# Optimization experiments

Measured on AMD Instinct MI355X. Metric: run time of the kernel, lower is better.

Reference implementation:

```python
import jax, jax.numpy as jnp
import numpy as np


def _proj(W, b, x):
    # 1x1 conv == per-pixel GEMM over channels: [O,C] x [B,C,H,W] -> [B,O,H,W]
    return jnp.einsum('oc,bchw->bohw', W, x) + b[None, :, None, None]


def _cross(src, ctx, Wq, bq, Wk, bk, Wv, bv):
    # queries from src, keys/values from ctx; returns [B,C,H,W]
    B, C, H, W = src.shape
    HW = H * W
    q = _proj(Wq, bq, src).reshape(B, -1, HW)   # [B, C//8, HW]
    k = _proj(Wk, bk, ctx).reshape(B, -1, HW)   # [B, C//8, HW]
    v = _proj(Wv, bv, ctx).reshape(B, C, HW)    # [B, C,    HW]
    # attn[b,i,j] = softmax_j( q[b,:,i] . k[b,:,j] )
    attn = jax.nn.softmax(jnp.einsum('bci,bcj->bij', q, k), axis=-1)
    out = jnp.einsum('bcj,bij->bci', v, attn)   # [B, C, HW]
    return out.reshape(B, C, H, W)


def setup_inputs() -> dict:
    key = jax.random.key(0)
    ks = jax.random.split(key, 8)
    dim = 256
    B, H, W = 4, 64, 64
    return {
        'x': jax.random.normal(ks[0], (B, dim, H, W), jnp.float32),
        'y': jax.random.normal(ks[1], (B, dim, H, W), jnp.float32),
        'Wq': jax.random.normal(ks[2], (dim // 8, dim), jnp.float32) * 0.05,
        'bq': jax.random.normal(ks[3], (dim // 8,), jnp.float32) * 0.05,
        'Wk': jax.random.normal(ks[4], (dim // 8, dim), jnp.float32) * 0.05,
        'bk': jax.random.normal(ks[5], (dim // 8,), jnp.float32) * 0.05,
        'Wv': jax.random.normal(ks[6], (dim, dim), jnp.float32) * 0.05,
        'bv': jax.random.normal(ks[7], (dim,), jnp.float32) * 0.05,
    }


def reference(x, y, Wq, bq, Wk, bk, Wv, bv):
    outx = _cross(x, y, Wq, bq, Wk, bk, Wv, bv)  # x queries attend to y
    outy = _cross(y, x, Wq, bq, Wk, bk, Wv, bv)  # y queries attend to x
    return (outx, outy)
```

## Files before the change

kernel.cpp:

```cpp
#include <hip/hip_runtime.h>

#define BB 4
#define CC 256
#define DD 32
#define SS 4096

typedef __bf16 bf16;
typedef __bf16 bf16x8 __attribute__((ext_vector_type(8)));
typedef __bf16 bf16x4 __attribute__((ext_vector_type(4)));
typedef float f32x4 __attribute__((ext_vector_type(4)));
typedef unsigned int u32;
typedef unsigned short u16;

#define Q_OFF  0
#define K_OFF  1048576
#define V_OFF  2097152
#define WB_OFF 10485760

static __device__ __forceinline__ u32 pack2(float lo, float hi) {
    bf16 a = (bf16)lo, b = (bf16)hi;
    u16 ua = __builtin_bit_cast(u16, a), ub = __builtin_bit_cast(u16, b);
    return (u32)ua | ((u32)ub << 16);
}

__global__ __launch_bounds__(256) void convert_w_kernel(
    const float* __restrict__ Wq, const float* __restrict__ Wk,
    const float* __restrict__ Wv, bf16* __restrict__ wb)
{
    const int gid = blockIdx.x*256 + threadIdx.x;
    const int idx = gid*8;
    const int o = idx >> 8, cc = idx & 255;
    const float* row = (o < 32) ? (Wq + (size_t)o*CC)
                     : (o < 64) ? (Wk + (size_t)(o-32)*CC)
                                : (Wv + (size_t)(o-64)*CC);
    const float4 a = *(const float4*)(row + cc);
    const float4 c = *(const float4*)(row + cc + 4);
    bf16x8 pk;
    pk[0]=(bf16)a.x; pk[1]=(bf16)a.y; pk[2]=(bf16)a.z; pk[3]=(bf16)a.w;
    pk[4]=(bf16)c.x; pk[5]=(bf16)c.y; pk[6]=(bf16)c.z; pk[7]=(bf16)c.w;
    *(bf16x8*)(wb + idx) = pk;
}

__global__ __launch_bounds__(256, 2) void proj_all_kernel(
    const float* __restrict__ x, const float* __restrict__ y,
    const bf16* __restrict__ wb,
    const float* __restrict__ bq, const float* __restrict__ bk,
    const float* __restrict__ bv,
    bf16* __restrict__ qout, bf16* __restrict__ kout, bf16* __restrict__ vout)
{
    __shared__ __align__(16) char smem[2*5120];
    bf16* xT  = (bf16*)smem;
    u32*  xTw = (u32*)smem;

    const int t    = threadIdx.x;
    const int lane = t & 63;
    const int w    = t >> 6;
    const int ln   = lane & 15;
    const int quad = lane >> 4;

    const int bid  = blockIdx.x;
    const int dirb = bid & 7;
    const int src  = dirb >> 2;
    const int b    = dirb & 3;
    const int i0   = (bid >> 3) * 64;
    const float* in = src ? y : x;
    const float* xbase = in + (size_t)b*CC*SS + i0;

    const int cp = t >> 4;
    const int pq = (t & 15) * 4;

    float bias[5];
    #pragma unroll
    for (int nbl = 0; nbl < 5; ++nbl) {
        const int o = 80*w + nbl*16 + ln;
        bias[nbl] = (o < 32) ? bq[o] : (o < 64) ? bk[o-32] : bv[o-64];
    }
    f32x4 acc[4][5];
    #pragma unroll
    for (int mb = 0; mb < 4; ++mb)
        #pragma unroll
        for (int nbl = 0; nbl < 5; ++nbl)
            acc[mb][nbl] = (f32x4){bias[nbl], bias[nbl], bias[nbl], bias[nbl]};

    const bf16* wrow = wb + (size_t)(80*w + ln)*CC + quad*8;
    bf16x8 bf[5];
    #pragma unroll
    for (int nbl = 0; nbl < 5; ++nbl)
        bf[nbl] = *(const bf16x8*)(wrow + (size_t)nbl*16*CC);

    {
        const float* r0 = xbase + (size_t)(2*cp)*SS + pq;
        const float4 a0 = *(const float4*)r0;
        const float4 a1 = *(const float4*)(r0 + SS);
        xTw[(pq+0)*20 + cp] = pack2(a0.x, a1.x);
        xTw[(pq+1)*20 + cp] = pack2(a0.y, a1.y);
        xTw[(pq+2)*20 + cp] = pack2(a0.z, a1.z);
        xTw[(pq+3)*20 + cp] = pack2(a0.w, a1.w);
    }
    float4 a0, a1;
    {
        const float* r1 = xbase + (size_t)(32 + 2*cp)*SS + pq;
        a0 = *(const float4*)r1;
        a1 = *(const float4*)(r1 + SS);
    }
    __syncthreads();

    for (int n = 0; n < 8; ++n) {
        bf16x8 af[4];
        #pragma unroll
        for (int mb = 0; mb < 4; ++mb)
            af[mb] = *(const bf16x8*)(xT + (n&1)*2560 + (mb*16 + ln)*40 + quad*8);
        if (n < 7) {
            u32* dst = xTw + ((n+1)&1)*1280;
            dst[(pq+0)*20 + cp] = pack2(a0.x, a1.x);
            dst[(pq+1)*20 + cp] = pack2(a0.y, a1.y);
            dst[(pq+2)*20 + cp] = pack2(a0.z, a1.z);
            dst[(pq+3)*20 + cp] = pack2(a0.w, a1.w);
        }
        {
            const int cc2 = ((n+2)*32) & 255;
            const float* r2 = xbase + (size_t)(cc2 + 2*cp)*SS + pq;
            a0 = *(const float4*)r2;
            a1 = *(const float4*)(r2 + SS);
        }
        #pragma unroll
        for (int mb = 0; mb < 4; ++mb)
            #pragma unroll
            for (int nbl = 0; nbl < 5; ++nbl)
                acc[mb][nbl] = __builtin_amdgcn_mfma_f32_16x16x32_bf16(
                                   af[mb], bf[nbl], acc[mb][nbl], 0, 0, 0);
        const int ccn = ((n+1)*32) & 255;
        #pragma unroll
        for (int nbl = 0; nbl < 5; ++nbl)
            bf[nbl] = *(const bf16x8*)(wrow + (size_t)nbl*16*CC + ccn);
        __syncthreads();
    }

    bf16* qo = qout + (size_t)(src*BB + b)*SS*DD;
    bf16* ko = kout + (size_t)(src*BB + b)*SS*DD;
    bf16* vo = vout + (size_t)(src*BB + b)*CC*SS;
    #pragma unroll
    for (int nbl = 0; nbl < 5; ++nbl) {
        const int o = 80*w + nbl*16 + ln;
        if (o < 32) {
            #pragma unroll
            for (int mb = 0; mb < 4; ++mb)
                #pragma unroll
                for (int r = 0; r < 4; ++r)
                    qo[(size_t)(i0 + mb*16 + quad*4 + r)*DD + o] = (bf16)acc[mb][nbl][r];
        } else if (o < 64) {
            #pragma unroll
            for (int mb = 0; mb < 4; ++mb)
                #pragma unroll
                for (int r = 0; r < 4; ++r)
                    ko[(size_t)(i0 + mb*16 + quad*4 + r)*DD + (o-32)] = (bf16)acc[mb][nbl][r];
        } else {
            const int c = o - 64;
            #pragma unroll
            for (int mb = 0; mb < 4; ++mb) {
                bf16x4 pk;
                #pragma unroll
                for (int r = 0; r < 4; ++r) pk[r] = (bf16)acc[mb][nbl][r];
                *(bf16x4*)(vo + (size_t)c*SS + i0 + mb*16 + quad*4) = pk;
            }
        }
    }
}

#define SM_M 16.0f

__global__ __launch_bounds__(256, 2) void attn_kernel(
    const bf16* __restrict__ qg, const bf16* __restrict__ kg,
    const bf16* __restrict__ vg, float* __restrict__ out)
{
    __shared__ __align__(16) char smem[18688];
    bf16*  p_s = (bf16*)smem;
    float* l_s = (float*)(smem + 18432);

    const int t    = threadIdx.x;
    const int lane = t & 63;
    const int w    = t >> 6;
    const int ln   = lane & 15;
    const int quad = lane >> 4;

    const int bid  = blockIdx.x;
    const int dirb = bid & 7;
    const int dir  = dirb >> 2;
    const int b    = dirb & 3;
    const int i0   = (bid >> 3) * 64;

    const bf16* q = qg + ((size_t)dir*BB + b)*SS*DD + (size_t)i0*DD;
    const bf16* k = kg + ((size_t)(1-dir)*BB + b)*SS*DD;
    const bf16* v = vg + ((size_t)(1-dir)*BB + b)*CC*SS;
    float* op = out + ((size_t)dir*BB + b)*CC*SS;

    const bf16x8 b_q = *(const bf16x8*)(q + (size_t)(w*16 + ln)*DD + quad*8);
    const bf16* kbase = k + (size_t)ln*DD + quad*8;
    const bf16* vptr[4];
    #pragma unroll
    for (int cb = 0; cb < 4; ++cb)
        vptr[cb] = v + (size_t)(w*64 + cb*16 + ln)*SS + quad*8;

    f32x4 o[4][4];
    #pragma unroll
    for (int qb = 0; qb < 4; ++qb)
        #pragma unroll
        for (int cb = 0; cb < 4; ++cb) o[qb][cb] = (f32x4){0.f,0.f,0.f,0.f};
    float lp = 0.f;

    bf16x8 kf[4], vf[2][4];
    #pragma unroll
    for (int nb = 0; nb < 4; ++nb)
        kf[nb] = *(const bf16x8*)(kbase + (size_t)(nb*16)*DD);
    #pragma unroll
    for (int ks = 0; ks < 2; ++ks)
        #pragma unroll
        for (int cb = 0; cb < 4; ++cb)
            vf[ks][cb] = *(const bf16x8*)(vptr[cb] + ks*32);

    {
        f32x4 s[4];
        #pragma unroll
        for (int nb = 0; nb < 4; ++nb)
            s[nb] = __builtin_amdgcn_mfma_f32_16x16x32_bf16(
                        kf[nb], b_q, (f32x4){0.f,0.f,0.f,0.f}, 0, 0, 0);
        #pragma unroll
        for (int nb = 0; nb < 4; ++nb)
            kf[nb] = *(const bf16x8*)(kbase + (size_t)(64 + nb*16)*DD);
        #pragma unroll
        for (int nb = 0; nb < 4; ++nb) {
            bf16x4 pk;
            #pragma unroll
            for (int r = 0; r < 4; ++r) {
                const float e = __expf(fminf(s[nb][r] - SM_M, 60.0f));
                lp += e;
                pk[r] = (bf16)e;
            }
            *(bf16x4*)(p_s + (w*16 + ln)*72 + nb*16 + quad*4) = pk;
        }
    }

    for (int n = 0; n < 64; ++n) {
        __syncthreads();
        const bf16* pr = p_s + (n & 1)*4608;
        bf16* pw = p_s + ((n + 1) & 1)*4608;

        f32x4 s[4];
        if (n < 63) {
            #pragma unroll
            for (int nb = 0; nb < 4; ++nb)
                s[nb] = __builtin_amdgcn_mfma_f32_16x16x32_bf16(
                            kf[nb], b_q, (f32x4){0.f,0.f,0.f,0.f}, 0, 0, 0);
            const int j2 = ((n + 2) << 6) & (SS - 1);
            #pragma unroll
            for (int nb = 0; nb < 4; ++nb)
                kf[nb] = *(const bf16x8*)(kbase + (size_t)(j2 + nb*16)*DD);
        }

        #pragma unroll
        for (int ks = 0; ks < 2; ++ks) {
            bf16x8 ap[4];
            #pragma unroll
            for (int qb = 0; qb < 4; ++qb)
                ap[qb] = *(const bf16x8*)(pr + (qb*16 + ln)*72 + ks*32 + quad*8);
            #pragma unroll
            for (int qb = 0; qb < 4; ++qb)
                #pragma unroll
                for (int cb = 0; cb < 4; ++cb)
                    o[qb][cb] = __builtin_amdgcn_mfma_f32_16x16x32_bf16(
                                    ap[qb], vf[ks][cb], o[qb][cb], 0, 0, 0);
        }
        const int j1 = ((n + 1) << 6) & (SS - 1);
        #pragma unroll
        for (int ks = 0; ks < 2; ++ks)
            #pragma unroll
            for (int cb = 0; cb < 4; ++cb)
                vf[ks][cb] = *(const bf16x8*)(vptr[cb] + j1 + ks*32);

        if (n < 63) {
            #pragma unroll
            for (int nb = 0; nb < 4; ++nb) {
                bf16x4 pk;
                #pragma unroll
                for (int r = 0; r < 4; ++r) {
                    const float e = __expf(fminf(s[nb][r] - SM_M, 60.0f));
                    lp += e;
                    pk[r] = (bf16)e;
                }
                *(bf16x4*)(pw + (w*16 + ln)*72 + nb*16 + quad*4) = pk;
            }
        }
    }

    lp += __shfl_xor(lp, 16);
    lp += __shfl_xor(lp, 32);
    if (lane < 16) l_s[w*16 + ln] = lp;
    __syncthreads();

    #pragma unroll
    for (int qb = 0; qb < 4; ++qb) {
        const f32x4 lq = *(const f32x4*)(l_s + qb*16 + quad*4);
        const float ri0 = 1.0f/lq[0], ri1 = 1.0f/lq[1], ri2 = 1.0f/lq[2], ri3 = 1.0f/lq[3];
        #pragma unroll
        for (int cb = 0; cb < 4; ++cb) {
            const int c = w*64 + cb*16 + ln;
            float4 val = make_float4(o[qb][cb][0]*ri0, o[qb][cb][1]*ri1,
                                     o[qb][cb][2]*ri2, o[qb][cb][3]*ri3);
            *(float4*)(op + (size_t)c*SS + i0 + qb*16 + quad*4) = val;
        }
    }
}

extern "C" void kernel_launch(void* const* d_in, const int* in_sizes, int n_in,
                              void* d_out, int out_size, void* d_ws, size_t ws_size,
                              hipStream_t stream)
{
    const float* x  = (const float*)d_in[0];
    const float* y  = (const float*)d_in[1];
    const float* Wq = (const float*)d_in[2];
    const float* bq = (const float*)d_in[3];
    const float* Wk = (const float*)d_in[4];
    const float* bk = (const float*)d_in[5];
    const float* Wv = (const float*)d_in[6];
    const float* bv = (const float*)d_in[7];
    float* out = (float*)d_out;
    bf16* ws   = (bf16*)d_ws;

    bf16* qw = ws + Q_OFF;
    bf16* kw = ws + K_OFF;
    bf16* vw = ws + V_OFF;
    bf16* wb = ws + WB_OFF;

    convert_w_kernel<<<40,  256, 0, stream>>>(Wq, Wk, Wv, wb);
    proj_all_kernel <<<512, 256, 0, stream>>>(x, y, wb, bq, bk, bv, qw, kw, vw);
    attn_kernel     <<<512, 256, 0, stream>>>(qw, kw, vw, out);
}
```

Before: 253.3 us.

## Double-buffer V fragments and replace syncthreads with lgkmcnt-only barrier

The attention loop is unrolled by two with ping-pong V register buffers, so the next V tile's global loads are issued at the start of each iteration instead of after the PV MFMAs. This gives those loads a full iteration of latency hiding. __syncthreads is replaced with a custom barrier that waits only on LDS and scalar counters (lgkmcnt), not on outstanding global loads, so in-flight prefetches are not drained at each barrier. The cost is extra VGPRs for the second V buffer, which could spill or hurt occupancy under launch_bounds(256,2).

```diff
diff --git a/kernel.cpp b/kernel.cpp
--- a/kernel.cpp
+++ b/kernel.cpp
@@ -11,6 +11,8 @@
 typedef float f32x4 __attribute__((ext_vector_type(4)));
 typedef unsigned int u32;
 typedef unsigned short u16;
+
+#define BAR() asm volatile("s_waitcnt lgkmcnt(0)\n\ts_barrier" ::: "memory")
 
 #define Q_OFF  0
 #define K_OFF  1048576
@@ -103,7 +105,7 @@
         a0 = *(const float4*)r1;
         a1 = *(const float4*)(r1 + SS);
     }
-    __syncthreads();
+    BAR();
 
     for (int n = 0; n < 8; ++n) {
         bf16x8 af[4];
@@ -133,7 +135,7 @@
         #pragma unroll
         for (int nbl = 0; nbl < 5; ++nbl)
             bf[nbl] = *(const bf16x8*)(wrow + (size_t)nbl*16*CC + ccn);
-        __syncthreads();
+        BAR();
     }
 
     bf16* qo = qout + (size_t)(src*BB + b)*SS*DD;
@@ -168,6 +170,56 @@
 }
 
 #define SM_M 16.0f
+
+#define ATTN_ITER(NN, VCUR, VNXT, PRBUF, PWBUF)                               \
+  {                                                                           \
+    BAR();                                                                    \
+    const int jn1 = ((NN + 1) << 6) & (SS - 1);                               \
+    if ((NN) < 63) {                                                          \
+      _Pragma("unroll")                                                       \
+      for (int ks = 0; ks < 2; ++ks)                                          \
+        _Pragma("unroll")                                                     \
+        for (int cb = 0; cb < 4; ++cb)                                        \
+          VNXT[ks][cb] = *(const bf16x8*)(vptr[cb] + jn1 + ks*32);            \
+    }                                                                         \
+    f32x4 s[4];                                                               \
+    if ((NN) < 63) {                                                          \
+      _Pragma("unroll")                                                       \
+      for (int nb = 0; nb < 4; ++nb)                                          \
+        s[nb] = __builtin_amdgcn_mfma_f32_16x16x32_bf16(kf[nb], b_q,          \
+                    (f32x4){0.f,0.f,0.f,0.f}, 0, 0, 0);                       \
+      const int j2 = ((NN + 2) << 6) & (SS - 1);                              \
+      _Pragma("unroll")                                                       \
+      for (int nb = 0; nb < 4; ++nb)                                          \
+        kf[nb] = *(const bf16x8*)(kbase + (size_t)(j2 + nb*16)*DD);           \
+    }                                                                         \
+    _Pragma("unroll")                                                         \
+    for (int ks = 0; ks < 2; ++ks) {                                          \
+      bf16x8 ap[4];                                                           \
+      _Pragma("unroll")                                                       \
+      for (int qb = 0; qb < 4; ++qb)                                          \
+        ap[qb] = *(const bf16x8*)(PRBUF + (qb*16 + ln)*72 + ks*32 + quad*8);  \
+      _Pragma("unroll")                                                       \
+      for (int qb = 0; qb < 4; ++qb)                                          \
+        _Pragma("unroll")                                                     \
+        for (int cb = 0; cb < 4; ++cb)                                        \
+          o[qb][cb] = __builtin_amdgcn_mfma_f32_16x16x32_bf16(                \
+                          ap[qb], VCUR[ks][cb], o[qb][cb], 0, 0, 0);          \
+    }                                                                         \
+    if ((NN) < 63) {                                                          \
+      _Pragma("unroll")                                                       \
+      for (int nb = 0; nb < 4; ++nb) {                                        \
+        bf16x4 pk;                                                            \
+        _Pragma("unroll")                                                     \
+        for (int r = 0; r < 4; ++r) {                                         \
+          const float e = __expf(fminf(s[nb][r] - SM_M, 60.0f));              \
+          lp += e;                                                            \
+          pk[r] = (bf16)e;                                                    \
+        }                                                                     \
+        *(bf16x4*)(PWBUF + (w*16 + ln)*72 + nb*16 + quad*4) = pk;             \
+      }                                                                       \
+    }                                                                         \
+  }
 
 __global__ __launch_bounds__(256, 2) void attn_kernel(
     const bf16* __restrict__ qg, const bf16* __restrict__ kg,
@@ -208,7 +260,7 @@
         for (int cb = 0; cb < 4; ++cb) o[qb][cb] = (f32x4){0.f,0.f,0.f,0.f};
     float lp = 0.f;
 
-    bf16x8 kf[4], vf[2][4];
+    bf16x8 kf[4], vfA[2][4], vfB[2][4];
     #pragma unroll
     for (int nb = 0; nb < 4; ++nb)
         kf[nb] = *(const bf16x8*)(kbase + (size_t)(nb*16)*DD);
@@ -216,7 +268,10 @@
     for (int ks = 0; ks < 2; ++ks)
         #pragma unroll
         for (int cb = 0; cb < 4; ++cb)
-            vf[ks][cb] = *(const bf16x8*)(vptr[cb] + ks*32);
+            vfA[ks][cb] = *(const bf16x8*)(vptr[cb] + ks*32);
+
+    bf16* pbuf0 = p_s;
+    bf16* pbuf1 = p_s + 4608;
 
     {
         f32x4 s[4];
@@ -236,60 +291,13 @@
                 lp += e;
                 pk[r] = (bf16)e;
             }
-            *(bf16x4*)(p_s + (w*16 + ln)*72 + nb*16 + quad*4) = pk;
-        }
-    }
-
-    for (int n = 0; n < 64; ++n) {
-        __syncthreads();
-        const bf16* pr = p_s + (n & 1)*4608;
-        bf16* pw = p_s + ((n + 1) & 1)*4608;
-
-        f32x4 s[4];
-        if (n < 63) {
-            #pragma unroll
-            for (int nb = 0; nb < 4; ++nb)
-                s[nb] = __builtin_amdgcn_mfma_f32_16x16x32_bf16(
-                            kf[nb], b_q, (f32x4){0.f,0.f,0.f,0.f}, 0, 0, 0);
-            const int j2 = ((n + 2) << 6) & (SS - 1);
-            #pragma unroll
-            for (int nb = 0; nb < 4; ++nb)
-                kf[nb] = *(const bf16x8*)(kbase + (size_t)(j2 + nb*16)*DD);
-        }
-
-        #pragma unroll
-        for (int ks = 0; ks < 2; ++ks) {
-            bf16x8 ap[4];
-            #pragma unroll
-            for (int qb = 0; qb < 4; ++qb)
-                ap[qb] = *(const bf16x8*)(pr + (qb*16 + ln)*72 + ks*32 + quad*8);
-            #pragma unroll
-            for (int qb = 0; qb < 4; ++qb)
-                #pragma unroll
-                for (int cb = 0; cb < 4; ++cb)
-                    o[qb][cb] = __builtin_amdgcn_mfma_f32_16x16x32_bf16(
-                                    ap[qb], vf[ks][cb], o[qb][cb], 0, 0, 0);
-        }
-        const int j1 = ((n + 1) << 6) & (SS - 1);
-        #pragma unroll
-        for (int ks = 0; ks < 2; ++ks)
-            #pragma unroll
-            for (int cb = 0; cb < 4; ++cb)
-                vf[ks][cb] = *(const bf16x8*)(vptr[cb] + j1 + ks*32);
-
-        if (n < 63) {
-            #pragma unroll
-            for (int nb = 0; nb < 4; ++nb) {
-                bf16x4 pk;
-                #pragma unroll
-                for (int r = 0; r < 4; ++r) {
-                    const float e = __expf(fminf(s[nb][r] - SM_M, 60.0f));
-                    lp += e;
-                    pk[r] = (bf16)e;
-                }
-                *(bf16x4*)(pw + (w*16 + ln)*72 + nb*16 + quad*4) = pk;
-            }
-        }
+            *(bf16x4*)(pbuf0 + (w*16 + ln)*72 + nb*16 + quad*4) = pk;
+        }
+    }
+
+    for (int n = 0; n < 64; n += 2) {
+        ATTN_ITER(n,     vfA, vfB, pbuf0, pbuf1)
+        ATTN_ITER(n + 1, vfB, vfA, pbuf1, pbuf0)
     }
 
     lp += __shfl_xor(lp, 16);
```

Result: no change. 256.8 us (+1.4%).

## Split attention key range across two wave groups and halve projection tiles

Applied to the files above, without the earlier changes.

The attention kernel now runs 512 threads per block, with two groups of four waves each handling half of the key/value sequence. The partial outputs and row sums are combined through shared memory at the end, which raises per-CU parallelism and latency hiding. The projection kernel uses 32-pixel tiles with twice as many blocks and a higher occupancy bound. A custom barrier that waits only on LDS counters replaces __syncthreads. The V fragment loads are no longer prefetched a step ahead, and the extra reduction adds shared-memory traffic and barriers.

```diff
diff --git a/kernel.cpp b/kernel.cpp
--- a/kernel.cpp
+++ b/kernel.cpp
@@ -11,6 +11,8 @@
 typedef float f32x4 __attribute__((ext_vector_type(4)));
 typedef unsigned int u32;
 typedef unsigned short u16;
+
+#define BAR() asm volatile("s_waitcnt lgkmcnt(0)\n\ts_barrier" ::: "memory")
 
 #define Q_OFF  0
 #define K_OFF  1048576
@@ -41,14 +43,14 @@
     *(bf16x8*)(wb + idx) = pk;
 }
 
-__global__ __launch_bounds__(256, 2) void proj_all_kernel(
+__global__ __launch_bounds__(256, 4) void proj_all_kernel(
     const float* __restrict__ x, const float* __restrict__ y,
     const bf16* __restrict__ wb,
     const float* __restrict__ bq, const float* __restrict__ bk,
     const float* __restrict__ bv,
     bf16* __restrict__ qout, bf16* __restrict__ kout, bf16* __restrict__ vout)
 {
-    __shared__ __align__(16) char smem[2*5120];
+    __shared__ __align__(16) char smem[2*2560];
     bf16* xT  = (bf16*)smem;
     u32*  xTw = (u32*)smem;
 
@@ -62,12 +64,12 @@
     const int dirb = bid & 7;
     const int src  = dirb >> 2;
     const int b    = dirb & 3;
-    const int i0   = (bid >> 3) * 64;
+    const int i0   = (bid >> 3) * 32;
     const float* in = src ? y : x;
     const float* xbase = in + (size_t)b*CC*SS + i0;
 
     const int cp = t >> 4;
-    const int pq = (t & 15) * 4;
+    const int pp = t & 15;
 
     float bias[5];
     #pragma unroll
@@ -75,9 +77,9 @@
         const int o = 80*w + nbl*16 + ln;
         bias[nbl] = (o < 32) ? bq[o] : (o < 64) ? bk[o-32] : bv[o-64];
     }
-    f32x4 acc[4][5];
-    #pragma unroll
-    for (int mb = 0; mb < 4; ++mb)
+    f32x4 acc[2][5];
+    #pragma unroll
+    for (int mb = 0; mb < 2; ++mb)
         #pragma unroll
         for (int nbl = 0; nbl < 5; ++nbl)
             acc[mb][nbl] = (f32x4){bias[nbl], bias[nbl], bias[nbl], bias[nbl]};
@@ -88,43 +90,36 @@
     for (int nbl = 0; nbl < 5; ++nbl)
         bf[nbl] = *(const bf16x8*)(wrow + (size_t)nbl*16*CC);
 
+    const float* xr = xbase + (size_t)(2*cp)*SS + 2*pp;
+
     {
-        const float* r0 = xbase + (size_t)(2*cp)*SS + pq;
-        const float4 a0 = *(const float4*)r0;
-        const float4 a1 = *(const float4*)(r0 + SS);
-        xTw[(pq+0)*20 + cp] = pack2(a0.x, a1.x);
-        xTw[(pq+1)*20 + cp] = pack2(a0.y, a1.y);
-        xTw[(pq+2)*20 + cp] = pack2(a0.z, a1.z);
-        xTw[(pq+3)*20 + cp] = pack2(a0.w, a1.w);
-    }
-    float4 a0, a1;
-    {
-        const float* r1 = xbase + (size_t)(32 + 2*cp)*SS + pq;
-        a0 = *(const float4*)r1;
-        a1 = *(const float4*)(r1 + SS);
-    }
-    __syncthreads();
+        const float2 r0 = *(const float2*)xr;
+        const float2 r1 = *(const float2*)(xr + SS);
+        xTw[(2*pp+0)*20 + cp] = pack2(r0.x, r1.x);
+        xTw[(2*pp+1)*20 + cp] = pack2(r0.y, r1.y);
+    }
+    float2 pa, pb;
+    pa = *(const float2*)(xr + (size_t)32*SS);
+    pb = *(const float2*)(xr + (size_t)33*SS);
+    BAR();
 
     for (int n = 0; n < 8; ++n) {
-        bf16x8 af[4];
-        #pragma unroll
-        for (int mb = 0; mb < 4; ++mb)
-            af[mb] = *(const bf16x8*)(xT + (n&1)*2560 + (mb*16 + ln)*40 + quad*8);
+        bf16x8 af[2];
+        #pragma unroll
+        for (int mb = 0; mb < 2; ++mb)
+            af[mb] = *(const bf16x8*)(xT + (n&1)*1280 + (mb*16 + ln)*40 + quad*8);
         if (n < 7) {
-            u32* dst = xTw + ((n+1)&1)*1280;
-            dst[(pq+0)*20 + cp] = pack2(a0.x, a1.x);
-            dst[(pq+1)*20 + cp] = pack2(a0.y, a1.y);
-            dst[(pq+2)*20 + cp] = pack2(a0.z, a1.z);
-            dst[(pq+3)*20 + cp] = pack2(a0.w, a1.w);
+            u32* dst = xTw + ((n+1)&1)*640;
+            dst[(2*pp+0)*20 + cp] = pack2(pa.x, pb.x);
+            dst[(2*pp+1)*20 + cp] = pack2(pa.y, pb.y);
         }
         {
-            const int cc2 = ((n+2)*32) & 255;
-            const float* r2 = xbase + (size_t)(cc2 + 2*cp)*SS + pq;
-            a0 = *(const float4*)r2;
-            a1 = *(const float4*)(r2 + SS);
-        }
-        #pragma unroll
-        for (int mb = 0; mb < 4; ++mb)
+            const size_t cc2 = (size_t)(((n+2)*32) & 255);
+            pa = *(const float2*)(xr + cc2*SS);
+            pb = *(const float2*)(xr + (cc2+1)*SS);
+        }
+        #pragma unroll
+        for (int mb = 0; mb < 2; ++mb)
             #pragma unroll
             for (int nbl = 0; nbl < 5; ++nbl)
                 acc[mb][nbl] = __builtin_amdgcn_mfma_f32_16x16x32_bf16(
@@ -133,7 +128,7 @@
         #pragma unroll
         for (int nbl = 0; nbl < 5; ++nbl)
             bf[nbl] = *(const bf16x8*)(wrow + (size_t)nbl*16*CC + ccn);
-        __syncthreads();
+        BAR();
     }
 
     bf16* qo = qout + (size_t)(src*BB + b)*SS*DD;
@@ -144,20 +139,20 @@
         const int o = 80*w + nbl*16 + ln;
         if (o < 32) {
             #pragma unroll
-            for (int mb = 0; mb < 4; ++mb)
+            for (int mb = 0; mb < 2; ++mb)
                 #pragma unroll
                 for (int r = 0; r < 4; ++r)
                     qo[(size_t)(i0 + mb*16 + quad*4 + r)*DD + o] = (bf16)acc[mb][nbl][r];
         } else if (o < 64) {
             #pragma unroll
-            for (int mb = 0; mb < 4; ++mb)
+            for (int mb = 0; mb < 2; ++mb)
                 #pragma unroll
                 for (int r = 0; r < 4; ++r)
                     ko[(size_t)(i0 + mb*16 + quad*4 + r)*DD + (o-32)] = (bf16)acc[mb][nbl][r];
         } else {
             const int c = o - 64;
             #pragma unroll
-            for (int mb = 0; mb < 4; ++mb) {
+            for (int mb = 0; mb < 2; ++mb) {
                 bf16x4 pk;
                 #pragma unroll
                 for (int r = 0; r < 4; ++r) pk[r] = (bf16)acc[mb][nbl][r];
@@ -169,17 +164,20 @@
 
 #define SM_M 16.0f
 
-__global__ __launch_bounds__(256, 2) void attn_kernel(
+__global__ __launch_bounds__(512, 4) void attn_kernel(
     const bf16* __restrict__ qg, const bf16* __restrict__ kg,
     const bf16* __restrict__ vg, float* __restrict__ out)
 {
-    __shared__ __align__(16) char smem[18688];
+    __shared__ __align__(16) char smem[37376];
     bf16*  p_s = (bf16*)smem;
-    float* l_s = (float*)(smem + 18432);
+    float* l_s = (float*)(smem + 36864);
+    float* s_o = (float*)smem;
 
     const int t    = threadIdx.x;
     const int lane = t & 63;
     const int w    = t >> 6;
+    const int g    = w >> 2;
+    const int wl   = w & 3;
     const int ln   = lane & 15;
     const int quad = lane >> 4;
 
@@ -194,12 +192,15 @@
     const bf16* v = vg + ((size_t)(1-dir)*BB + b)*CC*SS;
     float* op = out + ((size_t)dir*BB + b)*CC*SS;
 
-    const bf16x8 b_q = *(const bf16x8*)(q + (size_t)(w*16 + ln)*DD + quad*8);
+    const bf16x8 b_q = *(const bf16x8*)(q + (size_t)(wl*16 + ln)*DD + quad*8);
     const bf16* kbase = k + (size_t)ln*DD + quad*8;
     const bf16* vptr[4];
     #pragma unroll
     for (int cb = 0; cb < 4; ++cb)
-        vptr[cb] = v + (size_t)(w*64 + cb*16 + ln)*SS + quad*8;
+        vptr[cb] = v + (size_t)(wl*64 + cb*16 + ln)*SS + quad*8;
+
+    const int jbase = g * 2048;
+    bf16* pg = p_s + g*9216;
 
     f32x4 o[4][4];
     #pragma unroll
@@ -208,15 +209,10 @@
         for (int cb = 0; cb < 4; ++cb) o[qb][cb] = (f32x4){0.f,0.f,0.f,0.f};
     float lp = 0.f;
 
-    bf16x8 kf[4], vf[2][4];
+    bf16x8 kf[4];
     #pragma unroll
     for (int nb = 0; nb < 4; ++nb)
-        kf[nb] = *(const bf16x8*)(kbase + (size_t)(nb*16)*DD);
-    #pragma unroll
-    for (int ks = 0; ks < 2; ++ks)
-        #pragma unroll
-        for (int cb = 0; cb < 4; ++cb)
-            vf[ks][cb] = *(const bf16x8*)(vptr[cb] + ks*32);
+        kf[nb] = *(const bf16x8*)(kbase + (size_t)(jbase + nb*16)*DD);
 
     {
         f32x4 s[4];
@@ -226,7 +222,7 @@
                         kf[nb], b_q, (f32x4){0.f,0.f,0.f,0.f}, 0, 0, 0);
         #pragma unroll
         for (int nb = 0; nb < 4; ++nb)
-            kf[nb] = *(const bf16x8*)(kbase + (size_t)(64 + nb*16)*DD);
+            kf[nb] = *(const bf16x8*)(kbase + (size_t)(jbase + 64 + nb*16)*DD);
         #pragma unroll
         for (int nb = 0; nb < 4; ++nb) {
             bf16x4 pk;
@@ -236,33 +232,40 @@
                 lp += e;
                 pk[r] = (bf16)e;
             }
-            *(bf16x4*)(p_s + (w*16 + ln)*72 + nb*16 + quad*4) = pk;
-        }
-    }
-
-    for (int n = 0; n < 64; ++n) {
-        __syncthreads();
-        const bf16* pr = p_s + (n & 1)*4608;
-        bf16* pw = p_s + ((n + 1) & 1)*4608;
+            *(bf16x4*)(pg + (wl*16 + ln)*72 + nb*16 + quad*4) = pk;
+        }
+    }
+
+    for (int n = 0; n < 32; ++n) {
+        BAR();
+        const int j0 = jbase + (n << 6);
+
+        bf16x8 vf[2][4];
+        #pragma unroll
+        for (int ks = 0; ks < 2; ++ks)
+            #pragma unroll
+            for (int cb = 0; cb < 4; ++cb)
+                vf[ks][cb] = *(const bf16x8*)(vptr[cb] + j0 + ks*32);
 
         f32x4 s[4];
-        if (n < 63) {
+        if (n < 31) {
             #pragma unroll
             for (int nb = 0; nb < 4; ++nb)
                 s[nb] = __builtin_amdgcn_mfma_f32_16x16x32_bf16(
                             kf[nb], b_q, (f32x4){0.f,0.f,0.f,0.f}, 0, 0, 0);
-            const int j2 = ((n + 2) << 6) & (SS - 1);
+            const int j2 = (j0 + 128) & (SS - 1);
             #pragma unroll
             for (int nb = 0; nb < 4; ++nb)
                 kf[nb] = *(const bf16x8*)(kbase + (size_t)(j2 + nb*16)*DD);
         }
 
+        const bf16* prb = pg + (n & 1)*4608;
         #pragma unroll
         for (int ks = 0; ks < 2; ++ks) {
             bf16x8 ap[4];
             #pragma unroll
             for (int qb = 0; qb < 4; ++qb)
-                ap[qb] = *(const bf16x8*)(pr + (qb*16 + ln)*72 + ks*32 + quad*8);
+                ap[qb] = *(const bf16x8*)(prb + (qb*16 + ln)*72 + ks*32 + quad*8);
             #pragma unroll
             for (int qb = 0; qb < 4; ++qb)
                 #pragma unroll
@@ -270,14 +273,9 @@
                     o[qb][cb] = __builtin_amdgcn_mfma_f32_16x16x32_bf16(
                                     ap[qb], vf[ks][cb], o[qb][cb], 0, 0, 0);
         }
-        const int j1 = ((n + 1) << 6) & (SS - 1);
-        #pragma unroll
-        for (int ks = 0; ks < 2; ++ks)
-            #pragma unroll
-            for (int cb = 0; cb < 4; ++cb)
-                vf[ks][cb] = *(const bf16x8*)(vptr[cb] + j1 + ks*32);
-
-        if (n < 63) {
+
+        if (n < 31) {
+            bf16* pwb = pg + ((n + 1) & 1)*4608;
             #pragma unroll
             for (int nb = 0; nb < 4; ++nb) {
                 bf16x4 pk;
@@ -287,27 +285,53 @@
                     lp += e;
                     pk[r] = (bf16)e;
                 }
-                *(bf16x4*)(pw + (w*16 + ln)*72 + nb*16 + quad*4) = pk;
+                *(bf16x4*)(pwb + (wl*16 + ln)*72 + nb*16 + quad*4) = pk;
             }
         }
     }
 
     lp += __shfl_xor(lp, 16);
     lp += __shfl_xor(lp, 32);
-    if (lane < 16) l_s[w*16 + ln] = lp;
+    if (lane < 16) l_s[g*64 + wl*16 + ln] = lp;
     __syncthreads();
 
     #pragma unroll
-    for (int qb = 0; qb < 4; ++qb) {
-        const f32x4 lq = *(const f32x4*)(l_s + qb*16 + quad*4);
-        const float ri0 = 1.0f/lq[0], ri1 = 1.0f/lq[1], ri2 = 1.0f/lq[2], ri3 = 1.0f/lq[3];
-        #pragma unroll
-        for (int cb = 0; cb < 4; ++cb) {
-            const int c = w*64 + cb*16 + ln;
-            float4 val = make_float4(o[qb][cb][0]*ri0, o[qb][cb][1]*ri1,
-                                     o[qb][cb][2]*ri2, o[qb][cb][3]*ri3);
-            *(float4*)(op + (size_t)c*SS + i0 + qb*16 + quad*4) = val;
-        }
+    for (int h = 0; h < 2; ++h) {
+        if (g == 1) {
+            #pragma unroll
+            for (int hb = 0; hb < 2; ++hb) {
+                const int qb = 2*h + hb;
+                #pragma unroll
+                for (int cb = 0; cb < 4; ++cb) {
+                    const int c = wl*64 + cb*16 + ln;
+                    *(f32x4*)(s_o + ((hb*256 + c)*16 + quad*4)) = o[qb][cb];
+                }
+            }
+        }
+        __syncthreads();
+        if (g == 0) {
+            #pragma unroll
+            for (int hb = 0; hb < 2; ++hb) {
+                const int qb = 2*h + hb;
+                float rinv[4];
+                #pragma unroll
+                for (int r = 0; r < 4; ++r) {
+                    const int qi = qb*16 + quad*4 + r;
+                    rinv[r] = 1.0f / (l_s[qi] + l_s[64 + qi]);
+                }
+                #pragma unroll
+                for (int cb = 0; cb < 4; ++cb) {
+                    const int c = wl*64 + cb*16 + ln;
+                    const f32x4 o1 = *(const f32x4*)(s_o + ((hb*256 + c)*16 + quad*4));
+                    float4 val = make_float4((o[qb][cb][0] + o1[0])*rinv[0],
+                                             (o[qb][cb][1] + o1[1])*rinv[1],
+                                             (o[qb][cb][2] + o1[2])*rinv[2],
+                                             (o[qb][cb][3] + o1[3])*rinv[3]);
+                    *(float4*)(op + (size_t)c*SS + i0 + qb*16 + quad*4) = val;
+                }
+            }
+        }
+        __syncthreads();
     }
 }
 
@@ -331,7 +355,7 @@
     bf16* vw = ws + V_OFF;
     bf16* wb = ws + WB_OFF;
 
-    convert_w_kernel<<<40,  256, 0, stream>>>(Wq, Wk, Wv, wb);
-    proj_all_kernel <<<512, 256, 0, stream>>>(x, y, wb, bq, bk, bv, qw, kw, vw);
-    attn_kernel     <<<512, 256, 0, stream>>>(qw, kw, vw, out);
-}
+    convert_w_kernel<<<40,   256, 0, stream>>>(Wq, Wk, Wv, wb);
+    proj_all_kernel <<<1024, 256, 0, stream>>>(x, y, wb, bq, bk, bv, qw, kw, vw);
+    attn_kernel     <<<512,  512, 0, stream>>>(qw, kw, vw, out);
+}
```

Result: slower. 319.8 us (+26.2%).
